# Performance work log

Hardware: AMD Instinct MI355X
Metric: run time of the kernel (lower is better)

The kernel has to match this reference:

```python
import jax, jax.numpy as jnp
import numpy as np

B, C, H, W = 8, 384, 32, 32
NH, DK, DV = 8, 48, 48
CFF = 4 * C
L = H * W
NBIAS = (2 * H - 1) * (2 * W - 1)
LN_EPS = 1e-5


def _relative_indices(height, width):
    # rel_idx[q, k] = (gy_k - gy_q + H) * W + (gx_k - gx_q + W), matching the torch loop
    gy, gx = np.meshgrid(np.arange(height), np.arange(width), indexing='ij')
    gy = gy.ravel(); gx = gx.ravel()
    rel = (gy[None, :] - gy[:, None] + height) * width + (gx[None, :] - gx[:, None] + width)
    return jnp.asarray(rel, dtype=jnp.int64)


def setup_inputs() -> dict:
    key = jax.random.key(0)
    ks = jax.random.split(key, 10)
    s = 0.02  # small init scale
    return {
        'x': jax.random.normal(ks[0], (B, C, H, W), dtype=jnp.float32),
        'gamma': jnp.ones((C,), jnp.float32),
        'beta': jnp.zeros((C,), jnp.float32),
        'Wq': jax.random.normal(ks[1], (NH * DK, C), jnp.float32) * s,
        'Wk': jax.random.normal(ks[2], (NH * DK, C), jnp.float32) * s,
        'Wv': jax.random.normal(ks[3], (NH * DV, C), jnp.float32) * s,
        'Wo': jax.random.normal(ks[4], (C, NH * DV), jnp.float32) * s,
        'bo': jnp.zeros((C,), jnp.float32),
        'rel_bias': jax.random.normal(ks[5], (NH, NBIAS), jnp.float32),
        'fc1_w': jax.random.normal(ks[6], (CFF, C), jnp.float32) * s,
        'fc1_b': jnp.zeros((CFF,), jnp.float32),
        'fc2_w': jax.random.normal(ks[7], (C, CFF), jnp.float32) * s,
        'fc2_b': jnp.zeros((C,), jnp.float32),
        'rel_idx': _relative_indices(H, W),
    }


def reference(x, gamma, beta, Wq, Wk, Wv, Wo, bo, rel_bias,
              fc1_w, fc1_b, fc2_w, fc2_b, rel_idx):
    b, c, h_sp, w_sp = x.shape
    l = h_sp * w_sp
    nh = rel_bias.shape[0]
    dk = Wq.shape[0] // nh
    dv = Wv.shape[0] // nh

    # LayerNorm over channel dim (NHWC), then flatten to tokens [b, l, c]
    t = jnp.transpose(x, (0, 2, 3, 1))
    mu = jnp.mean(t, axis=-1, keepdims=True)
    var = jnp.mean(jnp.square(t - mu), axis=-1, keepdims=True)
    t = (t - mu) / jnp.sqrt(var + LN_EPS) * gamma + beta
    tok = t.reshape(b, l, c)

    q = (tok @ Wq.T).reshape(b, l, nh, dk)
    k = (tok @ Wk.T).reshape(b, l, nh, dk)
    v = (tok @ Wv.T).reshape(b, l, nh, dv)

    # gathered relative position bias: [nh, l, l]
    bias = rel_bias[:, rel_idx]
    # note: original applies NO 1/sqrt(d_k) scaling
    scores = jnp.einsum('blhd,bmhd->bhlm', q, k) + bias[None]
    attn = jax.nn.softmax(scores, axis=-1)
    out = jnp.einsum('bhlm,bmhd->blhd', attn, v).reshape(b, l, nh * dv)
    out = out @ Wo.T + bo  # [b, l, c]
    out = jnp.transpose(out, (0, 2, 1)).reshape(b, c, h_sp, w_sp)

    y = x + out  # attention residual (x_stem = x, no downsampling)

    # FFN: 1x1 convs == per-pixel linear over channels; exact (erf) gelu as torch default
    u = jnp.einsum('bchw,oc->bohw', y, fc1_w) + fc1_b[None, :, None, None]
    u = jax.nn.gelu(u, approximate=False)
    u = jnp.einsum('bchw,oc->bohw', u, fc2_w) + fc2_b[None, :, None, None]
    return y + u
```

## Files before the change

### kernel.cpp

```cpp
#include <hip/hip_runtime.h>
#include <math.h>

#define SL 1024
#define CH 384
#define NHEAD 8
#define DH 48
#define NBIAS 3969
#define NTOK 8192
#define BATCH 8
#define CFF 1536
#define LN_EPS 1e-5f
#define QKVLD 1152
#define HMS 3145728

#define WQKV_OFF 0
#define WO_OFF   442368
#define F1_OFF   589824
#define F2_OFF   1179648
#define WTOT     1769472

typedef float floatx4 __attribute__((ext_vector_type(4)));
typedef short bf16x8 __attribute__((ext_vector_type(8)));

__device__ __forceinline__ unsigned f2bf_u(float f) {
  unsigned u = __float_as_uint(f);
  return (u + 0x7fffu + ((u >> 16) & 1u)) >> 16;
}
__device__ __forceinline__ unsigned pack2(float a, float b) {
  return f2bf_u(a) | (f2bf_u(b) << 16);
}

__device__ __forceinline__ void gload_lds16(const void* g, void* l) {
  __builtin_amdgcn_global_load_lds(
      (const __attribute__((address_space(1))) void*)g,
      (__attribute__((address_space(3))) void*)l, 16, 0, 0);
}

__global__ void k_w2bf(const float* __restrict__ Wq, const float* __restrict__ Wk,
                       const float* __restrict__ Wv, const float* __restrict__ Wo,
                       const float* __restrict__ f1, const float* __restrict__ f2,
                       short* __restrict__ dst) {
  size_t i = ((size_t)blockIdx.x * 256 + threadIdx.x) * 8;
  if (i >= WTOT) return;
  const float* s;
  size_t base;
  if (i < 147456)        { s = Wq; base = 0; }
  else if (i < 294912)   { s = Wk; base = 147456; }
  else if (i < WO_OFF)   { s = Wv; base = 294912; }
  else if (i < F1_OFF)   { s = Wo; base = WO_OFF; }
  else if (i < F2_OFF)   { s = f1; base = F1_OFF; }
  else                   { s = f2; base = F2_OFF; }
  const float4* p = (const float4*)(s + (i - base));
  float4 a = p[0], b = p[1];
  uint4 o;
  o.x = pack2(a.x, a.y); o.y = pack2(a.z, a.w);
  o.z = pack2(b.x, b.y); o.w = pack2(b.z, b.w);
  *(uint4*)(dst + i) = o;
}

__global__ __launch_bounds__(256) void k_ln_fused(
    const float* __restrict__ x, const float* __restrict__ gamma,
    const float* __restrict__ beta, short* __restrict__ tok) {
  __shared__ float sx[32][385];
  int b = blockIdx.y, l0 = blockIdx.x * 32;
  int tid = threadIdx.x;
  const float* xb = x + (size_t)b * CH * SL;
  int cr = tid >> 3, ls = (tid & 7) * 4;
#pragma unroll
  for (int c0 = 0; c0 < CH; c0 += 32) {
    int c = c0 + cr;
    float4 v = *(const float4*)(xb + (size_t)c * SL + l0 + ls);
    sx[ls + 0][c] = v.x; sx[ls + 1][c] = v.y;
    sx[ls + 2][c] = v.z; sx[ls + 3][c] = v.w;
  }
  __syncthreads();
  int tl = tid >> 3, p = tid & 7;
  float vals[48];
  float s = 0.f, q = 0.f;
#pragma unroll
  for (int i = 0; i < 48; i++) {
    float v = sx[tl][p * 48 + i];
    vals[i] = v; s += v; q += v * v;
  }
  s += __shfl_xor(s, 1, 64); q += __shfl_xor(q, 1, 64);
  s += __shfl_xor(s, 2, 64); q += __shfl_xor(q, 2, 64);
  s += __shfl_xor(s, 4, 64); q += __shfl_xor(q, 4, 64);
  float mu = s * (1.0f / CH);
  float rstd = rsqrtf(q * (1.0f / CH) - mu * mu + LN_EPS);
  short* orow = tok + (size_t)(b * SL + l0 + tl) * CH + p * 48;
#pragma unroll
  for (int i = 0; i < 48; i += 2) {
    float a = (vals[i] - mu) * rstd * gamma[p * 48 + i] + beta[p * 48 + i];
    float c = (vals[i + 1] - mu) * rstd * gamma[p * 48 + i + 1] + beta[p * 48 + i + 1];
    *(unsigned*)(orow + i) = pack2(a, c);
  }
}

template <int BM, bool GELU, bool HAS_BIAS, int RES_MODE, int OUT_MODE>
__global__ __launch_bounds__(256) void k_gemm_mfma(
    const short* __restrict__ A, const short* __restrict__ W,
    const float* __restrict__ bias, const float* __restrict__ res,
    float* __restrict__ Cf, short* __restrict__ Cb, float* __restrict__ Ct,
    short* __restrict__ Chm, int N, int K) {
  constexpr int MI = BM / 32;
  constexpr int ASI = BM * 2 / 64;
  __shared__ short As[BM * 64];
  __shared__ short Bs[128 * 64];
  int tid = threadIdx.x;
  int wid = tid >> 6, lane = tid & 63;
  int lanelo = lane & 15, quad = lane >> 4;
  int wm = wid & 1, wn = wid >> 1;
  int m0 = blockIdx.y * BM, n0 = blockIdx.x * 128;

  const short* Aga[ASI];
  short* Ala[ASI];
#pragma unroll
  for (int s = 0; s < ASI; s++) {
    int p = wid * (BM * 2) + s * 64 + lane;
    int row = p >> 3, ch = (p & 7) ^ (row & 7);
    Aga[s] = A + (size_t)(m0 + row) * K + ch * 8;
    Ala[s] = As + (wid * (BM * 2) + s * 64) * 8;
  }
  const short* Bga[4];
  short* Bla[4];
#pragma unroll
  for (int s = 0; s < 4; s++) {
    int p = wid * 256 + s * 64 + lane;
    int row = p >> 3, ch = (p & 7) ^ (row & 7);
    Bga[s] = W + (size_t)(n0 + row) * K + ch * 8;
    Bla[s] = Bs + (wid * 256 + s * 64) * 8;
  }

  floatx4 acc[MI][4];
#pragma unroll
  for (int i = 0; i < MI; i++)
#pragma unroll
    for (int j = 0; j < 4; j++) acc[i][j] = {0.f, 0.f, 0.f, 0.f};

  int x8 = lanelo & 7;
  int ca0 = (quad ^ x8) * 8;
  int ca1 = ((quad + 4) ^ x8) * 8;

  for (int k0 = 0; k0 < K; k0 += 64) {
    __syncthreads();
#pragma unroll
    for (int s = 0; s < ASI; s++) gload_lds16(Aga[s] + k0, Ala[s]);
#pragma unroll
    for (int s = 0; s < 4; s++) gload_lds16(Bga[s] + k0, Bla[s]);
    __syncthreads();
#pragma unroll
    for (int h = 0; h < 2; h++) {
      int co = h ? ca1 : ca0;
      bf16x8 af[MI], bq[4];
#pragma unroll
      for (int i = 0; i < MI; i++)
        af[i] = *(const bf16x8*)&As[(wm * (BM / 2) + i * 16 + lanelo) * 64 + co];
#pragma unroll
      for (int j = 0; j < 4; j++)
        bq[j] = *(const bf16x8*)&Bs[(wn * 64 + j * 16 + lanelo) * 64 + co];
#pragma unroll
      for (int i = 0; i < MI; i++)
#pragma unroll
        for (int j = 0; j < 4; j++)
          acc[i][j] = __builtin_amdgcn_mfma_f32_16x16x32_bf16(af[i], bq[j], acc[i][j], 0, 0, 0);
    }
  }

  int colb = n0 + wn * 64 + lanelo;
  float bvv[4];
#pragma unroll
  for (int j = 0; j < 4; j++) bvv[j] = HAS_BIAS ? bias[colb + j * 16] : 0.0f;
#pragma unroll
  for (int i = 0; i < MI; i++) {
    int r = m0 + wm * (BM / 2) + i * 16 + quad * 4;
    int bb = r >> 10, ll = r & 1023;
#pragma unroll
    for (int j = 0; j < 4; j++) {
      int c = colb + j * 16;
      float4 rv = {0.f, 0.f, 0.f, 0.f};
      if (RES_MODE == 2) rv = *(const float4*)(res + ((size_t)bb * CH + c) * SL + ll);
      float vv[4];
#pragma unroll
      for (int reg = 0; reg < 4; reg++) {
        float v = acc[i][j][reg] + bvv[j];
        if (RES_MODE == 1) v += res[(size_t)(r + reg) * N + c];
        if (RES_MODE == 2) v += (&rv.x)[reg];
        if (GELU) v = 0.5f * v * (1.0f + erff(v * 0.7071067811865476f));
        vv[reg] = v;
      }
      if (OUT_MODE & 1) {
#pragma unroll
        for (int reg = 0; reg < 4; reg++) Cf[(size_t)(r + reg) * N + c] = vv[reg];
      }
      if (OUT_MODE & 2) {
#pragma unroll
        for (int reg = 0; reg < 4; reg++) Cb[(size_t)(r + reg) * N + c] = (short)f2bf_u(vv[reg]);
      }
      if (OUT_MODE & 4) {
        float4 ov = {vv[0], vv[1], vv[2], vv[3]};
        *(float4*)(Ct + ((size_t)bb * CH + c) * SL + ll) = ov;
      }
      if (OUT_MODE & 8) {
        int part = c / 384;
        int rem = c - part * 384;
        int hh = rem / 48, dd = rem - hh * 48;
        short* dst = Chm + (size_t)part * HMS +
                     ((size_t)(bb * NHEAD + hh) * SL + ll) * 48 + dd;
#pragma unroll
        for (int reg = 0; reg < 4; reg++) dst[reg * 48] = (short)f2bf_u(vv[reg]);
      }
    }
  }
}

__global__ __launch_bounds__(256) void k_attn_mfma(
    const short* __restrict__ qh, const short* __restrict__ kh,
    const short* __restrict__ vh, const float* __restrict__ rel_bias,
    short* __restrict__ ao) {
  __shared__ short QP[128 * 72];
  __shared__ short Ks[64 * 72];
  __shared__ short Vts[48 * 72];
  __shared__ float Bb[1152];

  int b = blockIdx.z, h = blockIdx.y;
  int l0 = blockIdx.x * 128;
  int tid = threadIdx.x;
  int wid = tid >> 6, lane = tid & 63;
  int lanelo = lane & 15, quad = lane >> 4;
  size_t hb = ((size_t)b * NHEAD + h) * SL;
  size_t bSL = (size_t)b * SL;
  const short* kbase = kh + hb * 48;
  const short* vbase = vh + hb * 48;

  {
    const short* qsrc = qh + (hb + l0) * 48;
#pragma unroll
    for (int s = 0; s < 3; s++) {
      int g = tid + 256 * s;
      int row = g / 6, pos = g - row * 6;
      *(uint4*)&QP[row * 72 + pos * 8] = *(const uint4*)(qsrc + g * 8);
    }
  }
  {
    const float* bsrc = rel_bias + h * NBIAS + (929 - l0);
    for (int j = tid; j < 1152; j += 256) Bb[j] = bsrc[j];
  }
  for (int z = tid; z < 128 * 8; z += 256) {
    int r = z >> 3, u = z & 7;
    ((unsigned*)&QP[r * 72 + 48])[u] = 0u;
    if (r < 64) ((unsigned*)&Ks[r * 72 + 48])[u] = 0u;
  }
  __syncthreads();

  bf16x8 aq[2][2];
#pragma unroll
  for (int i = 0; i < 2; i++) {
    aq[i][0] = *(const bf16x8*)&QP[(wid * 32 + i * 16 + lanelo) * 72 + quad * 8];
    aq[i][1] = *(const bf16x8*)&QP[(wid * 32 + i * 16 + lanelo) * 72 + 32 + quad * 8];
  }

  floatx4 O[2][3];
#pragma unroll
  for (int i = 0; i < 2; i++)
#pragma unroll
    for (int d = 0; d < 3; d++) O[i][d] = {0.f, 0.f, 0.f, 0.f};
  float lsum[2][4] = {{0.f, 0.f, 0.f, 0.f}, {0.f, 0.f, 0.f, 0.f}};
  int boffL[2];
#pragma unroll
  for (int i = 0; i < 2; i++)
    boffL[i] = 127 - (wid * 32 + i * 16 + quad * 4) + lanelo;

  int kg = 2 * tid;
  int krow = kg / 6, kpos = kg - krow * 6;
  int vmp = tid & 31, vdg = tid >> 5;

  short* Pw = &QP[wid * 32 * 72];

  for (int mt = 0; mt < SL; mt += 64) {
    __syncthreads();
    if (tid < 192) {
      const short* ksrc = kbase + (size_t)mt * 48 + kg * 8;
      *(uint4*)&Ks[krow * 72 + kpos * 8] = *(const uint4*)(ksrc);
      *(uint4*)&Ks[krow * 72 + (kpos + 1) * 8] = *(const uint4*)(ksrc + 8);
      const short* vs = vbase + (size_t)(mt + 2 * vmp) * 48 + vdg * 8;
      union { uint4 u; unsigned short s[8]; } va, vb;
      va.u = *(const uint4*)vs;
      vb.u = *(const uint4*)(vs + 48);
#pragma unroll
      for (int i = 0; i < 8; i++) {
        unsigned pk = (unsigned)va.s[i] | ((unsigned)vb.s[i] << 16);
        *(unsigned*)&Vts[(vdg * 8 + i) * 72 + 2 * vmp] = pk;
      }
    }
    __syncthreads();

    bf16x8 kb[4][2];
#pragma unroll
    for (int nt = 0; nt < 4; nt++) {
      kb[nt][0] = *(const bf16x8*)&Ks[(nt * 16 + lanelo) * 72 + quad * 8];
      kb[nt][1] = *(const bf16x8*)&Ks[(nt * 16 + lanelo) * 72 + 32 + quad * 8];
    }

#pragma unroll
    for (int i = 0; i < 2; i++) {
      floatx4 s[4];
#pragma unroll
      for (int nt = 0; nt < 4; nt++) {
        floatx4 a = {0.f, 0.f, 0.f, 0.f};
        a = __builtin_amdgcn_mfma_f32_16x16x32_bf16(aq[i][0], kb[nt][0], a, 0, 0, 0);
        a = __builtin_amdgcn_mfma_f32_16x16x32_bf16(aq[i][1], kb[nt][1], a, 0, 0, 0);
        s[nt] = a;
      }
#pragma unroll
      for (int nt = 0; nt < 4; nt++) {
        int mo = mt + nt * 16;
#pragma unroll
        for (int reg = 0; reg < 4; reg++) {
          float e = __expf(s[nt][reg] + Bb[boffL[i] - reg + mo]);
          lsum[i][reg] += e;
          Pw[(i * 16 + quad * 4 + reg) * 72 + nt * 16 + lanelo] = (short)f2bf_u(e);
        }
      }
    }
    __asm__ volatile("s_waitcnt lgkmcnt(0)" ::: "memory");
    bf16x8 pa[2][2];
#pragma unroll
    for (int i = 0; i < 2; i++) {
      pa[i][0] = *(const bf16x8*)&Pw[(i * 16 + lanelo) * 72 + quad * 8];
      pa[i][1] = *(const bf16x8*)&Pw[(i * 16 + lanelo) * 72 + 32 + quad * 8];
    }
#pragma unroll
    for (int d = 0; d < 3; d++) {
      bf16x8 v0 = *(const bf16x8*)&Vts[(d * 16 + lanelo) * 72 + quad * 8];
      bf16x8 v1 = *(const bf16x8*)&Vts[(d * 16 + lanelo) * 72 + 32 + quad * 8];
#pragma unroll
      for (int i = 0; i < 2; i++) {
        O[i][d] = __builtin_amdgcn_mfma_f32_16x16x32_bf16(pa[i][0], v0, O[i][d], 0, 0, 0);
        O[i][d] = __builtin_amdgcn_mfma_f32_16x16x32_bf16(pa[i][1], v1, O[i][d], 0, 0, 0);
      }
    }
  }

#pragma unroll
  for (int i = 0; i < 2; i++)
#pragma unroll
    for (int reg = 0; reg < 4; reg++) {
      float s = lsum[i][reg];
      s += __shfl_xor(s, 1, 64);
      s += __shfl_xor(s, 2, 64);
      s += __shfl_xor(s, 4, 64);
      s += __shfl_xor(s, 8, 64);
      float inv = 1.0f / s;
      size_t base =
          (bSL + (size_t)(l0 + wid * 32 + i * 16 + quad * 4 + reg)) * CH + h * DH;
      ao[base + 0 + lanelo]  = (short)f2bf_u(O[i][0][reg] * inv);
      ao[base + 16 + lanelo] = (short)f2bf_u(O[i][1][reg] * inv);
      ao[base + 32 + lanelo] = (short)f2bf_u(O[i][2][reg] * inv);
    }
}

extern "C" void kernel_launch(void* const* d_in, const int* in_sizes, int n_in,
                              void* d_out, int out_size, void* d_ws, size_t ws_size,
                              hipStream_t stream) {
  const float* x = (const float*)d_in[0];
  const float* gamma = (const float*)d_in[1];
  const float* beta = (const float*)d_in[2];
  const float* Wq = (const float*)d_in[3];
  const float* Wk = (const float*)d_in[4];
  const float* Wv = (const float*)d_in[5];
  const float* Wo = (const float*)d_in[6];
  const float* bo = (const float*)d_in[7];
  const float* rel_bias = (const float*)d_in[8];
  const float* fc1_w = (const float*)d_in[9];
  const float* fc1_b = (const float*)d_in[10];
  const float* fc2_w = (const float*)d_in[11];
  const float* fc2_b = (const float*)d_in[12];
  float* out = (float*)d_out;

  const size_t TOKCH = (size_t)NTOK * CH;
  float* ws_f = (float*)d_ws;
  float* yb = ws_f;
  short* wbf    = (short*)(yb + TOKCH);
  short* tok_bf = wbf + WTOT;
  short* hm     = tok_bf + TOKCH;
  short* ao_bf  = hm + 3 * (size_t)HMS;
  short* yb_bf  = ao_bf + TOKCH;
  short* h1_bf  = yb_bf + TOKCH;

  k_w2bf<<<WTOT / 8 / 256, 256, 0, stream>>>(Wq, Wk, Wv, Wo, fc1_w, fc2_w, wbf);
  k_ln_fused<<<dim3(SL / 32, BATCH), 256, 0, stream>>>(x, gamma, beta, tok_bf);

  k_gemm_mfma<128, false, false, 0, 8>
      <<<dim3(QKVLD / 128, NTOK / 128), 256, 0, stream>>>(
          tok_bf, wbf + WQKV_OFF, nullptr, nullptr, nullptr, nullptr, nullptr,
          hm, QKVLD, CH);

  k_attn_mfma<<<dim3(SL / 128, NHEAD, BATCH), 256, 0, stream>>>(
      hm, hm + HMS, hm + 2 * (size_t)HMS, rel_bias, ao_bf);

  k_gemm_mfma<64, false, true, 2, 3>
      <<<dim3(CH / 128, NTOK / 64), 256, 0, stream>>>(
          ao_bf, wbf + WO_OFF, bo, x, yb, yb_bf, nullptr, nullptr, CH, CH);

  k_gemm_mfma<128, true, true, 0, 2>
      <<<dim3(CFF / 128, NTOK / 128), 256, 0, stream>>>(
          yb_bf, wbf + F1_OFF, fc1_b, nullptr, nullptr, h1_bf, nullptr, nullptr,
          CFF, CH);

  k_gemm_mfma<64, false, true, 1, 4>
      <<<dim3(CH / 128, NTOK / 64), 256, 0, stream>>>(
          h1_bf, wbf + F2_OFF, fc2_b, yb, nullptr, nullptr, out, nullptr, CH, CFF);
}
```

Before: 215.4 us.

## Split attention key range across two blocks and merge with a combine kernel

Each attention block now handles half of the key sequence, which doubles the grid from 512 to 1024 blocks. Each block writes unnormalised bf16 partial outputs and row sums to reused workspace, and a new combine kernel adds the two halves, normalises them and writes to the token layout. The softmax exponent now uses exp2f with a log2e-prescaled bias held in a smaller LDS buffer. The intent is better CU occupancy on the attention stage. The cost is an extra launch, extra round-trip traffic for the partial results, and an extra bf16 rounding of the partial outputs.

```diff
diff --git a/kernel.cpp b/kernel.cpp
--- a/kernel.cpp
+++ b/kernel.cpp
@@ -12,6 +12,7 @@
 #define LN_EPS 1e-5f
 #define QKVLD 1152
 #define HMS 3145728
+#define LOG2E 1.4426950408889634f
 
 #define WQKV_OFF 0
 #define WO_OFF   442368
@@ -28,6 +29,9 @@
 }
 __device__ __forceinline__ unsigned pack2(float a, float b) {
   return f2bf_u(a) | (f2bf_u(b) << 16);
+}
+__device__ __forceinline__ float bf2f(short s) {
+  return __uint_as_float(((unsigned)(unsigned short)s) << 16);
 }
 
 __device__ __forceinline__ void gload_lds16(const void* g, void* l) {
@@ -216,21 +220,22 @@
 __global__ __launch_bounds__(256) void k_attn_mfma(
     const short* __restrict__ qh, const short* __restrict__ kh,
     const short* __restrict__ vh, const float* __restrict__ rel_bias,
-    short* __restrict__ ao) {
+    short* __restrict__ op, float* __restrict__ ls) {
   __shared__ short QP[128 * 72];
   __shared__ short Ks[64 * 72];
   __shared__ short Vts[48 * 72];
-  __shared__ float Bb[1152];
+  __shared__ float Bb[640];
 
   int b = blockIdx.z, h = blockIdx.y;
-  int l0 = blockIdx.x * 128;
+  int ks = blockIdx.x & 1;
+  int l0 = (blockIdx.x >> 1) * 128;
+  int ms = ks * 512;
   int tid = threadIdx.x;
   int wid = tid >> 6, lane = tid & 63;
   int lanelo = lane & 15, quad = lane >> 4;
   size_t hb = ((size_t)b * NHEAD + h) * SL;
-  size_t bSL = (size_t)b * SL;
-  const short* kbase = kh + hb * 48;
-  const short* vbase = vh + hb * 48;
+  const short* kbase = kh + (hb + ms) * 48;
+  const short* vbase = vh + (hb + ms) * 48;
 
   {
     const short* qsrc = qh + (hb + l0) * 48;
@@ -242,8 +247,8 @@
     }
   }
   {
-    const float* bsrc = rel_bias + h * NBIAS + (929 - l0);
-    for (int j = tid; j < 1152; j += 256) Bb[j] = bsrc[j];
+    const float* bsrc = rel_bias + h * NBIAS + (929 - l0 + ms);
+    for (int j = tid; j < 640; j += 256) Bb[j] = bsrc[j] * LOG2E;
   }
   for (int z = tid; z < 128 * 8; z += 256) {
     int r = z >> 3, u = z & 7;
@@ -276,7 +281,7 @@
 
   short* Pw = &QP[wid * 32 * 72];
 
-  for (int mt = 0; mt < SL; mt += 64) {
+  for (int mt = 0; mt < 512; mt += 64) {
     __syncthreads();
     if (tid < 192) {
       const short* ksrc = kbase + (size_t)mt * 48 + kg * 8;
@@ -316,7 +321,7 @@
         int mo = mt + nt * 16;
 #pragma unroll
         for (int reg = 0; reg < 4; reg++) {
-          float e = __expf(s[nt][reg] + Bb[boffL[i] - reg + mo]);
+          float e = exp2f(fmaf(s[nt][reg], LOG2E, Bb[boffL[i] - reg + mo]));
           lsum[i][reg] += e;
           Pw[(i * 16 + quad * 4 + reg) * 72 + nt * 16 + lanelo] = (short)f2bf_u(e);
         }
@@ -341,6 +346,8 @@
     }
   }
 
+  size_t obase = (size_t)ks * HMS + hb * 48;
+  int lsbase = ks * (BATCH * NHEAD * SL) + (int)(hb);
 #pragma unroll
   for (int i = 0; i < 2; i++)
 #pragma unroll
@@ -350,13 +357,34 @@
       s += __shfl_xor(s, 2, 64);
       s += __shfl_xor(s, 4, 64);
       s += __shfl_xor(s, 8, 64);
-      float inv = 1.0f / s;
-      size_t base =
-          (bSL + (size_t)(l0 + wid * 32 + i * 16 + quad * 4 + reg)) * CH + h * DH;
-      ao[base + 0 + lanelo]  = (short)f2bf_u(O[i][0][reg] * inv);
-      ao[base + 16 + lanelo] = (short)f2bf_u(O[i][1][reg] * inv);
-      ao[base + 32 + lanelo] = (short)f2bf_u(O[i][2][reg] * inv);
-    }
+      int q = l0 + wid * 32 + i * 16 + quad * 4 + reg;
+      if (lanelo == 0) ls[lsbase + q] = s;
+      size_t base = obase + (size_t)q * 48;
+      op[base + 0 + lanelo]  = (short)f2bf_u(O[i][0][reg]);
+      op[base + 16 + lanelo] = (short)f2bf_u(O[i][1][reg]);
+      op[base + 32 + lanelo] = (short)f2bf_u(O[i][2][reg]);
+    }
+}
+
+#define NROWS 65536
+__global__ __launch_bounds__(256) void k_attn_combine(
+    const short* __restrict__ op, const float* __restrict__ ls,
+    short* __restrict__ ao) {
+  int gid = blockIdx.x * 256 + threadIdx.x;
+  int row = gid / 6, ch = gid - row * 6;
+  float inv = 1.0f / (ls[row] + ls[NROWS + row]);
+  bf16x8 va = *(const bf16x8*)(op + (size_t)row * 48 + ch * 8);
+  bf16x8 vb = *(const bf16x8*)(op + (size_t)HMS + (size_t)row * 48 + ch * 8);
+  int b = row >> 13, h = (row >> 10) & 7, q = row & 1023;
+  short* dst = ao + ((size_t)(b << 10) + q) * CH + h * 48 + ch * 8;
+  unsigned outw[4];
+#pragma unroll
+  for (int j = 0; j < 4; j++) {
+    float a0 = bf2f(va[2 * j]), a1 = bf2f(va[2 * j + 1]);
+    float b0 = bf2f(vb[2 * j]), b1 = bf2f(vb[2 * j + 1]);
+    outw[j] = pack2((a0 + b0) * inv, (a1 + b1) * inv);
+  }
+  *(uint4*)dst = *(uint4*)outw;
 }
 
 extern "C" void kernel_launch(void* const* d_in, const int* in_sizes, int n_in,
@@ -386,6 +414,8 @@
   short* ao_bf  = hm + 3 * (size_t)HMS;
   short* yb_bf  = ao_bf + TOKCH;
   short* h1_bf  = yb_bf + TOKCH;
+  short* op  = h1_bf;
+  float* lsw = (float*)tok_bf;
 
   k_w2bf<<<WTOT / 8 / 256, 256, 0, stream>>>(Wq, Wk, Wv, Wo, fc1_w, fc2_w, wbf);
   k_ln_fused<<<dim3(SL / 32, BATCH), 256, 0, stream>>>(x, gamma, beta, tok_bf);
@@ -395,8 +425,9 @@
           tok_bf, wbf + WQKV_OFF, nullptr, nullptr, nullptr, nullptr, nullptr,
           hm, QKVLD, CH);
 
-  k_attn_mfma<<<dim3(SL / 128, NHEAD, BATCH), 256, 0, stream>>>(
-      hm, hm + HMS, hm + 2 * (size_t)HMS, rel_bias, ao_bf);
+  k_attn_mfma<<<dim3((SL / 128) * 2, NHEAD, BATCH), 256, 0, stream>>>(
+      hm, hm + HMS, hm + 2 * (size_t)HMS, rel_bias, op, lsw);
+  k_attn_combine<<<(NROWS * 6) / 256, 256, 0, stream>>>(op, lsw, ao_bf);
 
   k_gemm_mfma<64, false, true, 2, 3>
       <<<dim3(CH / 128, NTOK / 64), 256, 0, stream>>>(
```

After: 223.4 us. +3.7%, slower.

## Compute transposed scores to keep P in registers and skip LDS round-trip

Applied to the files above, without the earlier changes.

The QK^T MFMA is swapped to produce S^T, so each lane's accumulator already matches the B-operand layout of the PV MFMA. Probabilities are packed to bf16 in registers instead of being written to and reread from LDS. V is stored with a permuted column order to match, exp is rewritten as exp2 with the bias prescaled by log2e, and the output is staged through LDS for coalesced 16-byte global stores. The cost is extra operand reordering logic and more live registers for the V fragments.

```diff
diff --git a/kernel.cpp b/kernel.cpp
--- a/kernel.cpp
+++ b/kernel.cpp
@@ -12,6 +12,7 @@
 #define LN_EPS 1e-5f
 #define QKVLD 1152
 #define HMS 3145728
+#define LOG2E 1.4426950408889634f
 
 #define WQKV_OFF 0
 #define WO_OFF   442368
@@ -243,7 +244,7 @@
   }
   {
     const float* bsrc = rel_bias + h * NBIAS + (929 - l0);
-    for (int j = tid; j < 1152; j += 256) Bb[j] = bsrc[j];
+    for (int j = tid; j < 1152; j += 256) Bb[j] = bsrc[j] * LOG2E;
   }
   for (int z = tid; z < 128 * 8; z += 256) {
     int r = z >> 3, u = z & 7;
@@ -254,27 +255,27 @@
 
   bf16x8 aq[2][2];
 #pragma unroll
-  for (int i = 0; i < 2; i++) {
-    aq[i][0] = *(const bf16x8*)&QP[(wid * 32 + i * 16 + lanelo) * 72 + quad * 8];
-    aq[i][1] = *(const bf16x8*)&QP[(wid * 32 + i * 16 + lanelo) * 72 + 32 + quad * 8];
-  }
-
-  floatx4 O[2][3];
-#pragma unroll
-  for (int i = 0; i < 2; i++)
-#pragma unroll
-    for (int d = 0; d < 3; d++) O[i][d] = {0.f, 0.f, 0.f, 0.f};
-  float lsum[2][4] = {{0.f, 0.f, 0.f, 0.f}, {0.f, 0.f, 0.f, 0.f}};
-  int boffL[2];
-#pragma unroll
-  for (int i = 0; i < 2; i++)
-    boffL[i] = 127 - (wid * 32 + i * 16 + quad * 4) + lanelo;
+  for (int qi = 0; qi < 2; qi++) {
+    aq[qi][0] = *(const bf16x8*)&QP[(wid * 32 + qi * 16 + lanelo) * 72 + quad * 8];
+    aq[qi][1] = *(const bf16x8*)&QP[(wid * 32 + qi * 16 + lanelo) * 72 + 32 + quad * 8];
+  }
+
+  floatx4 O[3][2];
+#pragma unroll
+  for (int dt = 0; dt < 3; dt++)
+#pragma unroll
+    for (int qi = 0; qi < 2; qi++) O[dt][qi] = {0.f, 0.f, 0.f, 0.f};
+  float lsum[2] = {0.f, 0.f};
+  int boff[2];
+#pragma unroll
+  for (int qi = 0; qi < 2; qi++)
+    boff[qi] = 127 + quad * 4 - (wid * 32 + qi * 16 + lanelo);
 
   int kg = 2 * tid;
   int krow = kg / 6, kpos = kg - krow * 6;
   int vmp = tid & 31, vdg = tid >> 5;
-
-  short* Pw = &QP[wid * 32 * 72];
+  int kk = 2 * vmp;
+  int vcol = (kk & 3) + ((kk >> 2) & 3) * 8 + ((kk >> 4) & 1) * 4 + (kk >> 5) * 32;
 
   for (int mt = 0; mt < SL; mt += 64) {
     __syncthreads();
@@ -282,14 +283,14 @@
       const short* ksrc = kbase + (size_t)mt * 48 + kg * 8;
       *(uint4*)&Ks[krow * 72 + kpos * 8] = *(const uint4*)(ksrc);
       *(uint4*)&Ks[krow * 72 + (kpos + 1) * 8] = *(const uint4*)(ksrc + 8);
-      const short* vs = vbase + (size_t)(mt + 2 * vmp) * 48 + vdg * 8;
+      const short* vs = vbase + (size_t)(mt + kk) * 48 + vdg * 8;
       union { uint4 u; unsigned short s[8]; } va, vb;
       va.u = *(const uint4*)vs;
       vb.u = *(const uint4*)(vs + 48);
 #pragma unroll
       for (int i = 0; i < 8; i++) {
         unsigned pk = (unsigned)va.s[i] | ((unsigned)vb.s[i] << 16);
-        *(unsigned*)&Vts[(vdg * 8 + i) * 72 + 2 * vmp] = pk;
+        *(unsigned*)&Vts[(vdg * 8 + i) * 72 + vcol] = pk;
       }
     }
     __syncthreads();
@@ -300,63 +301,72 @@
       kb[nt][0] = *(const bf16x8*)&Ks[(nt * 16 + lanelo) * 72 + quad * 8];
       kb[nt][1] = *(const bf16x8*)&Ks[(nt * 16 + lanelo) * 72 + 32 + quad * 8];
     }
-
-#pragma unroll
-    for (int i = 0; i < 2; i++) {
-      floatx4 s[4];
+    bf16x8 vf[3][2];
+#pragma unroll
+    for (int dt = 0; dt < 3; dt++) {
+      vf[dt][0] = *(const bf16x8*)&Vts[(dt * 16 + lanelo) * 72 + quad * 8];
+      vf[dt][1] = *(const bf16x8*)&Vts[(dt * 16 + lanelo) * 72 + 32 + quad * 8];
+    }
+
+#pragma unroll
+    for (int qi = 0; qi < 2; qi++) {
+      floatx4 sc[4];
 #pragma unroll
       for (int nt = 0; nt < 4; nt++) {
         floatx4 a = {0.f, 0.f, 0.f, 0.f};
-        a = __builtin_amdgcn_mfma_f32_16x16x32_bf16(aq[i][0], kb[nt][0], a, 0, 0, 0);
-        a = __builtin_amdgcn_mfma_f32_16x16x32_bf16(aq[i][1], kb[nt][1], a, 0, 0, 0);
-        s[nt] = a;
-      }
+        a = __builtin_amdgcn_mfma_f32_16x16x32_bf16(kb[nt][0], aq[qi][0], a, 0, 0, 0);
+        a = __builtin_amdgcn_mfma_f32_16x16x32_bf16(kb[nt][1], aq[qi][1], a, 0, 0, 0);
+        sc[nt] = a;
+      }
+      unsigned pw[4][2];
 #pragma unroll
       for (int nt = 0; nt < 4; nt++) {
-        int mo = mt + nt * 16;
-#pragma unroll
-        for (int reg = 0; reg < 4; reg++) {
-          float e = __expf(s[nt][reg] + Bb[boffL[i] - reg + mo]);
-          lsum[i][reg] += e;
-          Pw[(i * 16 + quad * 4 + reg) * 72 + nt * 16 + lanelo] = (short)f2bf_u(e);
-        }
-      }
-    }
-    __asm__ volatile("s_waitcnt lgkmcnt(0)" ::: "memory");
-    bf16x8 pa[2][2];
-#pragma unroll
-    for (int i = 0; i < 2; i++) {
-      pa[i][0] = *(const bf16x8*)&Pw[(i * 16 + lanelo) * 72 + quad * 8];
-      pa[i][1] = *(const bf16x8*)&Pw[(i * 16 + lanelo) * 72 + 32 + quad * 8];
-    }
-#pragma unroll
-    for (int d = 0; d < 3; d++) {
-      bf16x8 v0 = *(const bf16x8*)&Vts[(d * 16 + lanelo) * 72 + quad * 8];
-      bf16x8 v1 = *(const bf16x8*)&Vts[(d * 16 + lanelo) * 72 + 32 + quad * 8];
-#pragma unroll
-      for (int i = 0; i < 2; i++) {
-        O[i][d] = __builtin_amdgcn_mfma_f32_16x16x32_bf16(pa[i][0], v0, O[i][d], 0, 0, 0);
-        O[i][d] = __builtin_amdgcn_mfma_f32_16x16x32_bf16(pa[i][1], v1, O[i][d], 0, 0, 0);
-      }
-    }
-  }
-
-#pragma unroll
-  for (int i = 0; i < 2; i++)
-#pragma unroll
-    for (int reg = 0; reg < 4; reg++) {
-      float s = lsum[i][reg];
-      s += __shfl_xor(s, 1, 64);
-      s += __shfl_xor(s, 2, 64);
-      s += __shfl_xor(s, 4, 64);
-      s += __shfl_xor(s, 8, 64);
-      float inv = 1.0f / s;
-      size_t base =
-          (bSL + (size_t)(l0 + wid * 32 + i * 16 + quad * 4 + reg)) * CH + h * DH;
-      ao[base + 0 + lanelo]  = (short)f2bf_u(O[i][0][reg] * inv);
-      ao[base + 16 + lanelo] = (short)f2bf_u(O[i][1][reg] * inv);
-      ao[base + 32 + lanelo] = (short)f2bf_u(O[i][2][reg] * inv);
-    }
+        int bidx = boff[qi] + mt + nt * 16;
+        float e0 = exp2f(fmaf(sc[nt][0], LOG2E, Bb[bidx + 0]));
+        float e1 = exp2f(fmaf(sc[nt][1], LOG2E, Bb[bidx + 1]));
+        float e2 = exp2f(fmaf(sc[nt][2], LOG2E, Bb[bidx + 2]));
+        float e3 = exp2f(fmaf(sc[nt][3], LOG2E, Bb[bidx + 3]));
+        lsum[qi] += (e0 + e1) + (e2 + e3);
+        pw[nt][0] = pack2(e0, e1);
+        pw[nt][1] = pack2(e2, e3);
+      }
+      union U8 { unsigned u[4]; bf16x8 v; };
+      U8 pb0, pb1;
+      pb0.u[0] = pw[0][0]; pb0.u[1] = pw[0][1]; pb0.u[2] = pw[1][0]; pb0.u[3] = pw[1][1];
+      pb1.u[0] = pw[2][0]; pb1.u[1] = pw[2][1]; pb1.u[2] = pw[3][0]; pb1.u[3] = pw[3][1];
+#pragma unroll
+      for (int dt = 0; dt < 3; dt++) {
+        O[dt][qi] = __builtin_amdgcn_mfma_f32_16x16x32_bf16(vf[dt][0], pb0.v, O[dt][qi], 0, 0, 0);
+        O[dt][qi] = __builtin_amdgcn_mfma_f32_16x16x32_bf16(vf[dt][1], pb1.v, O[dt][qi], 0, 0, 0);
+      }
+    }
+  }
+
+  float inv[2];
+#pragma unroll
+  for (int qi = 0; qi < 2; qi++) {
+    float s = lsum[qi];
+    s += __shfl_xor(s, 16, 64);
+    s += __shfl_xor(s, 32, 64);
+    inv[qi] = 1.0f / s;
+  }
+#pragma unroll
+  for (int dt = 0; dt < 3; dt++)
+#pragma unroll
+    for (int qi = 0; qi < 2; qi++) {
+      unsigned w0 = pack2(O[dt][qi][0] * inv[qi], O[dt][qi][1] * inv[qi]);
+      unsigned w1 = pack2(O[dt][qi][2] * inv[qi], O[dt][qi][3] * inv[qi]);
+      uint2 wv = {w0, w1};
+      *(uint2*)&QP[(wid * 32 + qi * 16 + lanelo) * 72 + dt * 16 + quad * 4] = wv;
+    }
+  __asm__ volatile("s_waitcnt lgkmcnt(0)" ::: "memory");
+#pragma unroll
+  for (int s = 0; s < 3; s++) {
+    int g = lane + 64 * s;
+    int qloc = g / 6, pos = g - qloc * 6;
+    uint4 val = *(const uint4*)&QP[(wid * 32 + qloc) * 72 + pos * 8];
+    *(uint4*)(ao + (bSL + (size_t)(l0 + wid * 32 + qloc)) * CH + h * DH + pos * 8) = val;
+  }
 }
 
 extern "C" void kernel_launch(void* const* d_in, const int* in_sizes, int n_in,
```

Result: no change. 215.4 us (+0.0%).
